# Kernel optimization log

Hardware: AMD Instinct MI355X
Metric: run time of the kernel (lower is better)

The kernel has to match this reference:

```python
import jax, jax.numpy as jnp
import numpy as np
from jax import lax

P = 32   # patch_size
D = 128  # emb_dim
E = 8    # num_experts
K = 2    # top-k
C = 3    # in_channels


def _conv(x, w, b, stride, groups, pad):
    y = lax.conv_general_dilated(
        x, w, (stride, stride), [(pad, pad), (pad, pad)],
        feature_group_count=groups,
        dimension_numbers=('NCHW', 'OIHW', 'NCHW'))
    return jax.nn.relu(y + b[None, :, None, None])


def setup_inputs() -> dict:
    key = jax.random.key(0)
    ks = jax.random.split(key, 16)
    s = 0.02
    inp = {
        'x': jax.random.normal(ks[0], (16, C, 512, 512), dtype=jnp.float32),
        'gate_w1': jax.random.normal(ks[1], (C * P * P, D), dtype=jnp.float32) * s,
        'gate_b1': jnp.zeros((D,), jnp.float32),
        'gate_w2': jax.random.normal(ks[2], (D, E), dtype=jnp.float32) * s,
        'gate_b2': jnp.zeros((E,), jnp.float32),
        'dw1_w': jax.random.normal(ks[3], (E, C, 1, 3, 3), dtype=jnp.float32) * s,
        'dw1_b': jnp.zeros((E, C), jnp.float32),
        'pw1_w': jax.random.normal(ks[4], (E, D, C, 1, 1), dtype=jnp.float32) * s,
        'pw1_b': jnp.zeros((E, D), jnp.float32),
        'dw2_w': jax.random.normal(ks[5], (E, D, 1, 3, 3), dtype=jnp.float32) * s,
        'dw2_b': jnp.zeros((E, D), jnp.float32),
        'pw2_w': jax.random.normal(ks[6], (E, D, D, 1, 1), dtype=jnp.float32) * s,
        'pw2_b': jnp.zeros((E, D), jnp.float32),
    }
    return inp


def reference(x, gate_w1, gate_b1, gate_w2, gate_b2,
              dw1_w, dw1_b, pw1_w, pw1_b, dw2_w, dw2_b, pw2_w, pw2_b):
    B, Cc, H, W = x.shape
    hp, wp = H // P, W // P
    N = hp * wp
    BN = B * N
    # nn.Unfold(kernel=stride=P) -> non-overlapping patches, (c,i,j) flatten order
    patches = x.reshape(B, Cc, hp, P, wp, P)
    patches = patches.transpose(0, 2, 4, 1, 3, 5).reshape(B, N, Cc * P * P)
    # gate MLP
    h = jax.nn.relu(patches @ gate_w1 + gate_b1)
    logits = h @ gate_w2 + gate_b2              # [B,N,E]
    topk_vals, topk_idx = lax.top_k(logits, K)  # sorted descending, like torch
    weights = jax.nn.softmax(topk_vals, axis=-1)
    patches_sp = patches.reshape(BN, Cc, P, P)
    # dense per-expert depthwise-separable conv stacks (small fixed loop over E)
    outs = []
    for e in range(E):
        y = _conv(patches_sp, dw1_w[e], dw1_b[e], 2, Cc, 1)  # [BN,C,16,16]
        y = _conv(y, pw1_w[e], pw1_b[e], 1, 1, 0)            # [BN,D,16,16]
        y = _conv(y, dw2_w[e], dw2_b[e], 2, D, 1)            # [BN,D,8,8]
        y = _conv(y, pw2_w[e], pw2_b[e], 1, 1, 0)            # [BN,D,8,8]
        outs.append(y.mean(axis=(2, 3)))                     # adaptive avg pool 1
    expert_outs = jnp.stack(outs, axis=1)                    # [BN,E,D]
    idx = topk_idx.reshape(BN, K)
    w = weights.reshape(BN, K)
    sel = jnp.take_along_axis(expert_outs, idx[:, :, None], axis=1)  # [BN,K,D]
    out = (w[:, :, None] * sel).sum(axis=1)                  # [BN,D]
    return out.reshape(B, hp, wp, D).transpose(0, 3, 1, 2)
```

## Files before the change

kernel.cpp:

```cpp
#include <hip/hip_runtime.h>

#define NPATCH 4096
#define NFRAG 49152

typedef __attribute__((ext_vector_type(8))) __bf16 bf16x8;
typedef __attribute__((ext_vector_type(4))) __bf16 bf16x4;
typedef __attribute__((ext_vector_type(4))) float f32x4;

__global__ __launch_bounds__(256) void prep_kernel(const float* __restrict__ pw2_w,
                                                   bf16x8* __restrict__ wpk) {
  int tid = blockIdx.x * 256 + threadIdx.x;
  int l = tid & 63, nt = (tid >> 6) & 7, kt = (tid >> 9) & 3, e = tid >> 11;
  int n = nt * 16 + (l & 15);
  int k = kt * 32 + (l >> 4) * 8;
  const float* src = &pw2_w[((size_t)(e * 128 + n)) * 128 + k];
  float4 a = *(const float4*)src;
  float4 b = *(const float4*)(src + 4);
  bf16x8 r = { (__bf16)a.x, (__bf16)a.y, (__bf16)a.z, (__bf16)a.w,
               (__bf16)b.x, (__bf16)b.y, (__bf16)b.z, (__bf16)b.w };
  wpk[tid] = r;
}

__global__ __launch_bounds__(256) void prep_w1(const float* __restrict__ w1,
                                               bf16x8* __restrict__ w1f) {
  int tid = blockIdx.x * 256 + threadIdx.x;
  int l = tid & 63, nt = (tid >> 6) & 7, ktg = tid >> 9;
  int k0 = ktg * 32 + (l >> 4) * 8, d = nt * 16 + (l & 15);
  bf16x8 h, lo;
#pragma unroll
  for (int j = 0; j < 8; ++j) {
    float v = w1[(size_t)(k0 + j) * 128 + d];
    __bf16 hv = (__bf16)v;
    h[j] = hv;
    lo[j] = (__bf16)(v - (float)hv);
  }
  w1f[tid] = h;
  w1f[NFRAG + tid] = lo;
}

__global__ __launch_bounds__(512) void gate_mfma(
    const float* __restrict__ x, const bf16x8* __restrict__ w1f,
    const float* __restrict__ b1, const float* __restrict__ w2,
    const float* __restrict__ b2, int* __restrict__ gidx,
    float* __restrict__ gw)
{
  __shared__ __bf16 Ah[2][8][64][8];
  __shared__ __bf16 Al[2][8][64][8];
  __shared__ float hs[16][128];
  __shared__ float ls[16][8];

  const int t  = threadIdx.x;
  const int p0 = blockIdx.x * 16;
  const int l  = t & 63;
  const int wv = t >> 6;
  const int mrow  = l & 15;
  const int kslot = l >> 4;

  const int sp   = l & 15;
  const int sj4  = (l >> 4) + 4 * (wv & 1);
  const int srr0 = (wv >> 1);
  const int srr1 = 4 + (wv >> 1);
  size_t pbase;
  {
    int gp = p0 + sp;
    int bb = gp >> 8, ph = (gp >> 4) & 15, pwc = gp & 15;
    pbase = ((size_t)(bb * 3) * 512 + ph * 32) * 512 + pwc * 32;
  }

  f32x4 accA[4], accB[4];
#pragma unroll
  for (int i = 0; i < 4; ++i) {
    accA[i] = (f32x4){0.f, 0.f, 0.f, 0.f};
    accB[i] = (f32x4){0.f, 0.f, 0.f, 0.f};
  }

#define SLOAD(ch, R0, R1) do {                                                      \
    R0 = *(const float4*)&x[pbase + (size_t)((ch) >> 2) * 262144 +                  \
                            (size_t)(((ch) & 3) * 8 + srr0) * 512 + sj4 * 4];       \
    R1 = *(const float4*)&x[pbase + (size_t)((ch) >> 2) * 262144 +                  \
                            (size_t)(((ch) & 3) * 8 + srr1) * 512 + sj4 * 4];       \
  } while (0)

#define SPLIT4(V, HP, LP) do {                                                      \
    bf16x4 h_, lo_;                                                                 \
    h_[0] = (__bf16)V.x; lo_[0] = (__bf16)(V.x - (float)h_[0]);                     \
    h_[1] = (__bf16)V.y; lo_[1] = (__bf16)(V.y - (float)h_[1]);                     \
    h_[2] = (__bf16)V.z; lo_[2] = (__bf16)(V.z - (float)h_[2]);                     \
    h_[3] = (__bf16)V.w; lo_[3] = (__bf16)(V.w - (float)h_[3]);                     \
    *(bf16x4*)(HP) = h_; *(bf16x4*)(LP) = lo_;                                      \
  } while (0)

#define SSTORE(ch, R0, R1) do {                                                     \
    const int bf_ = (ch) & 1;                                                       \
    SPLIT4(R0, &Ah[bf_][srr0][(sj4 >> 1) * 16 + sp][(sj4 & 1) * 4],                 \
               &Al[bf_][srr0][(sj4 >> 1) * 16 + sp][(sj4 & 1) * 4]);                \
    SPLIT4(R1, &Ah[bf_][srr1][(sj4 >> 1) * 16 + sp][(sj4 & 1) * 4],                 \
               &Al[bf_][srr1][(sj4 >> 1) * 16 + sp][(sj4 & 1) * 4]);                \
  } while (0)

#define BLOAD(ch, BH, BL) do {                                                      \
    const bf16x8* wp_ = w1f + (size_t)(ch) * 4096 + wv * 64 + l;                    \
    _Pragma("unroll")                                                               \
    for (int q = 0; q < 8; ++q) { BH[q] = wp_[q * 512]; BL[q] = wp_[NFRAG + q * 512]; } \
  } while (0)

#define MFMA_PASS(ch, BH, BL) do {                                                  \
    const int bf_ = (ch) & 1;                                                       \
    _Pragma("unroll")                                                               \
    for (int ktl = 0; ktl < 8; ++ktl) {                                             \
      bf16x8 ah_ = *(const bf16x8*)&Ah[bf_][ktl][l][0];                             \
      bf16x8 al_ = *(const bf16x8*)&Al[bf_][ktl][l][0];                             \
      const int r_ = ktl & 3;                                                       \
      accA[r_] = __builtin_amdgcn_mfma_f32_16x16x32_bf16(ah_, BH[ktl], accA[r_], 0, 0, 0); \
      accB[r_] = __builtin_amdgcn_mfma_f32_16x16x32_bf16(ah_, BL[ktl], accB[r_], 0, 0, 0); \
      accB[r_] = __builtin_amdgcn_mfma_f32_16x16x32_bf16(al_, BH[ktl], accB[r_], 0, 0, 0); \
    }                                                                               \
  } while (0)

  float4 r0, r1;
  bf16x8 bh0[8], bl0[8], bh1[8], bl1[8];

  SLOAD(0, r0, r1);
  BLOAD(0, bh0, bl0);
  SSTORE(0, r0, r1);
  __syncthreads();

#pragma unroll
  for (int cc = 0; cc < 12; cc += 2) {
    if (cc + 1 < 12) { SLOAD(cc + 1, r0, r1); BLOAD(cc + 1, bh1, bl1); }
    MFMA_PASS(cc, bh0, bl0);
    if (cc + 1 < 12) SSTORE(cc + 1, r0, r1);
    __syncthreads();
    if (cc + 2 < 12) { SLOAD(cc + 2, r0, r1); BLOAD(cc + 2, bh0, bl0); }
    MFMA_PASS(cc + 1, bh1, bl1);
    if (cc + 2 < 12) SSTORE(cc + 2, r0, r1);
    __syncthreads();
  }
#undef SLOAD
#undef SPLIT4
#undef SSTORE
#undef BLOAD
#undef MFMA_PASS

  {
    f32x4 sA = (accA[0] + accA[1]) + (accA[2] + accA[3]);
    f32x4 sB = (accB[0] + accB[1]) + (accB[2] + accB[3]);
    const int d = wv * 16 + mrow;
    const float bb1 = b1[d];
#pragma unroll
    for (int r = 0; r < 4; ++r) {
      int m = kslot * 4 + r;
      hs[m][d] = fmaxf(sA[r] + sB[r] + bb1, 0.f);
    }
  }
  __syncthreads();

  if (t < 128) {
    int p = t >> 3, e = t & 7;
    float s = 0.f;
    for (int d0 = 0; d0 < 128; d0 += 32) {
      float cs = 0.f;
#pragma unroll
      for (int dd = 0; dd < 32; ++dd)
        cs = fmaf(hs[p][d0 + dd], w2[(d0 + dd) * 8 + e], cs);
      s += cs;
    }
    ls[p][e] = s + b2[e];
  }
  __syncthreads();

  if (t < 16) {
    int gp = p0 + t;
    float v[8];
#pragma unroll
    for (int e = 0; e < 8; ++e) v[e] = ls[t][e];
    int e0 = 0;
#pragma unroll
    for (int e = 1; e < 8; ++e) if (v[e] > v[e0]) e0 = e;
    int e1 = (e0 == 0) ? 1 : 0;
#pragma unroll
    for (int e = 0; e < 8; ++e) { if (e != e0 && v[e] > v[e1]) e1 = e; }
    float bexp = expf(v[e1] - v[e0]);
    float inv  = 1.f / (1.f + bexp);
    gidx[gp * 2 + 0] = e0;
    gidx[gp * 2 + 1] = e1;
    gw[gp * 2 + 0] = inv;
    gw[gp * 2 + 1] = bexp * inv;
  }
}

__global__ __launch_bounds__(512, 4) void gate_kernel(
    const float* __restrict__ x, const float* __restrict__ w1,
    const float* __restrict__ b1, const float* __restrict__ w2,
    const float* __restrict__ b2, int* __restrict__ gidx,
    float* __restrict__ gw)
{
  __shared__ float As[8][1024];
  __shared__ float hs[8][128];
  __shared__ float ls[8][8];

  const int t   = threadIdx.x;
  const int p0  = blockIdx.x * 8;
  const int d   = t & 127;
  const int grp = t >> 7;
  const int pa  = grp * 2, pb = grp * 2 + 1;

  float acc0 = 0.f, acc1 = 0.f;

  for (int c = 0; c < 3; ++c) {
#pragma unroll
    for (int it = 0; it < 4; ++it) {
      int i = t + it * 512;
      int p = i >> 8, rem = i & 255, r = rem >> 3, j4 = (rem & 7) * 4;
      int gp = p0 + p;
      int bb = gp >> 8, ph = (gp >> 4) & 15, pwc = gp & 15;
      *(float4*)&As[p][r * 32 + j4] =
          *(const float4*)&x[((size_t)(bb * 3 + c) * 512 + ph * 32 + r) * 512 + pwc * 32 + j4];
    }
    __syncthreads();

    const float* wdp = w1 + (size_t)c * 131072 + d;
    for (int ch = 0; ch < 32; ++ch) {
      float bv[32];
#pragma unroll
      for (int j = 0; j < 32; ++j) bv[j] = wdp[(ch * 32 + j) * 128];
      const int kl = ch * 32;
      float ca = 0.f, cb = 0.f;
#pragma unroll
      for (int q = 0; q < 8; ++q) {
        float4 a0 = *(const float4*)&As[pa][kl + q * 4];
        float4 a1 = *(const float4*)&As[pb][kl + q * 4];
        ca = fmaf(a0.x, bv[q * 4 + 0], ca); ca = fmaf(a0.y, bv[q * 4 + 1], ca);
        ca = fmaf(a0.z, bv[q * 4 + 2], ca); ca = fmaf(a0.w, bv[q * 4 + 3], ca);
        cb = fmaf(a1.x, bv[q * 4 + 0], cb); cb = fmaf(a1.y, bv[q * 4 + 1], cb);
        cb = fmaf(a1.z, bv[q * 4 + 2], cb); cb = fmaf(a1.w, bv[q * 4 + 3], cb);
      }
      acc0 += ca; acc1 += cb;
    }
    __syncthreads();
  }

  hs[pa][d] = fmaxf(acc0 + b1[d], 0.f);
  hs[pb][d] = fmaxf(acc1 + b1[d], 0.f);
  __syncthreads();

  if (t < 64) {
    int p = t >> 3, e = t & 7;
    float s = 0.f;
    for (int d0 = 0; d0 < 128; d0 += 32) {
      float cs = 0.f;
#pragma unroll
      for (int dd = 0; dd < 32; ++dd)
        cs = fmaf(hs[p][d0 + dd], w2[(d0 + dd) * 8 + e], cs);
      s += cs;
    }
    ls[p][e] = s + b2[e];
  }
  __syncthreads();

  if (t < 8) {
    int gp = p0 + t;
    float v[8];
#pragma unroll
    for (int e = 0; e < 8; ++e) v[e] = ls[t][e];
    int e0 = 0;
#pragma unroll
    for (int e = 1; e < 8; ++e) if (v[e] > v[e0]) e0 = e;
    int e1 = (e0 == 0) ? 1 : 0;
#pragma unroll
    for (int e = 0; e < 8; ++e) { if (e != e0 && v[e] > v[e1]) e1 = e; }
    float bexp = expf(v[e1] - v[e0]);
    float inv  = 1.f / (1.f + bexp);
    gidx[gp * 2 + 0] = e0;
    gidx[gp * 2 + 1] = e1;
    gw[gp * 2 + 0] = inv;
    gw[gp * 2 + 1] = bexp * inv;
  }
}


#define EXPERT_COMMON_PRE                                                          \
  __shared__ float  ps[3][32][36];                                                 \
  __shared__ float  y1s[3][256];                                                   \
  __shared__ __bf16 y3b[64][140];                                                  \
  __shared__ float  posum[4][128];                                                 \
  __shared__ float  outbuf[128];                                                   \
  const int t  = threadIdx.x;                                                      \
  const int gp = blockIdx.x;                                                       \
  const int b = gp >> 8, ph = (gp >> 4) & 15, pw = gp & 15;                        \
  const int l = t & 63, wv = t >> 6;                                               \
  _Pragma("unroll")                                                                \
  for (int it = 0; it < 3; ++it) {                                                 \
    int f4i = t + 256 * it;                                                        \
    int c = f4i >> 8, r = (f4i >> 3) & 31, j4 = f4i & 7;                           \
    *(float4*)&ps[c][r][j4 * 4] =                                                  \
        *(const float4*)&x[((size_t)(b * 3 + c) * 512 + ph * 32 + r) * 512 +       \
                           pw * 32 + j4 * 4];                                      \
  }                                                                                \
  if (t < 128) outbuf[t] = 0.f;                                                    \
  const int dd   = t & 127;                                                        \
  const int half = t >> 7;                                                         \
  __syncthreads();

#define EXPERT_PHASES_1_2                                                          \
    for (int oi = t; oi < 768; oi += 256) {                                        \
      int c = oi >> 8, p = (oi >> 4) & 15, q = oi & 15;                            \
      float a = dw1_b[e * 3 + c];                                                  \
      const float* wp_ = &dw1_w[(e * 3 + c) * 9];                                  \
      _Pragma("unroll")                                                            \
      for (int di = 0; di < 3; ++di) {                                             \
        int ii = 2 * p + di - 1;                                                   \
        if (ii < 0) continue;                                                      \
        _Pragma("unroll")                                                          \
        for (int dj = 0; dj < 3; ++dj) {                                           \
          int jj = 2 * q + dj - 1;                                                 \
          if (jj < 0) continue;                                                    \
          a = fmaf(wp_[di * 3 + dj], ps[c][ii][jj], a);                            \
        }                                                                          \
      }                                                                            \
      y1s[c][p * 16 + q] = fmaxf(a, 0.f);                                          \
    }                                                                              \
    __syncthreads();                                                               \
    {                                                                              \
      const float pwa = pw1_w[(e * 128 + dd) * 3 + 0];                             \
      const float pwb = pw1_w[(e * 128 + dd) * 3 + 1];                             \
      const float pwc = pw1_w[(e * 128 + dd) * 3 + 2];                             \
      const float pb  = pw1_b[e * 128 + dd];                                       \
      float dwv[9];                                                                \
      _Pragma("unroll")                                                            \
      for (int i = 0; i < 9; ++i) dwv[i] = dw2_w[(e * 128 + dd) * 9 + i];          \
      const float db = dw2_b[e * 128 + dd];                                        \
      for (int u = half * 4; u < half * 4 + 4; ++u) {                              \
        float vacc[8];                                                             \
        _Pragma("unroll")                                                          \
        for (int v = 0; v < 8; ++v) vacc[v] = db;                                  \
        _Pragma("unroll")                                                          \
        for (int di = 0; di < 3; ++di) {                                           \
          int ii = 2 * u + di - 1;                                                 \
          if (ii < 0) continue;                                                    \
          float y2row[16];                                                         \
          _Pragma("unroll")                                                        \
          for (int q4 = 0; q4 < 4; ++q4) {                                         \
            float4 a  = *(const float4*)&y1s[0][ii * 16 + q4 * 4];                 \
            float4 bq = *(const float4*)&y1s[1][ii * 16 + q4 * 4];                 \
            float4 cq = *(const float4*)&y1s[2][ii * 16 + q4 * 4];                 \
            y2row[q4 * 4 + 0] = fmaxf(fmaf(pwa, a.x, fmaf(pwb, bq.x, fmaf(pwc, cq.x, pb))), 0.f); \
            y2row[q4 * 4 + 1] = fmaxf(fmaf(pwa, a.y, fmaf(pwb, bq.y, fmaf(pwc, cq.y, pb))), 0.f); \
            y2row[q4 * 4 + 2] = fmaxf(fmaf(pwa, a.z, fmaf(pwb, bq.z, fmaf(pwc, cq.z, pb))), 0.f); \
            y2row[q4 * 4 + 3] = fmaxf(fmaf(pwa, a.w, fmaf(pwb, bq.w, fmaf(pwc, cq.w, pb))), 0.f); \
          }                                                                        \
          _Pragma("unroll")                                                        \
          for (int v = 0; v < 8; ++v) {                                            \
            _Pragma("unroll")                                                      \
            for (int dj = 0; dj < 3; ++dj) {                                       \
              int jj = 2 * v + dj - 1;                                             \
              if (jj < 0) continue;                                                \
              vacc[v] = fmaf(dwv[di * 3 + dj], y2row[jj], vacc[v]);                \
            }                                                                      \
          }                                                                        \
        }                                                                          \
        _Pragma("unroll")                                                          \
        for (int v = 0; v < 8; ++v)                                                \
          y3b[u * 8 + v][dd] = (__bf16)fmaxf(vacc[v], 0.f);                        \
      }                                                                            \
    }

#define EXPERT_EPILOG                                                              \
    _Pragma("unroll")                                                              \
    for (int nt = 0; nt < 8; ++nt) {                                               \
      float bias = pw2_b[e * 128 + nt * 16 + (l & 15)];                            \
      float s = fmaxf(acc[nt][0] + bias, 0.f) + fmaxf(acc[nt][1] + bias, 0.f)      \
              + fmaxf(acc[nt][2] + bias, 0.f) + fmaxf(acc[nt][3] + bias, 0.f);     \
      s += __shfl_xor(s, 16);                                                      \
      s += __shfl_xor(s, 32);                                                      \
      if (l < 16) posum[wv][nt * 16 + l] = s;                                      \
    }

__global__ __launch_bounds__(256, 4) void expert_packed(
    const float* __restrict__ x,
    const float* __restrict__ dw1_w, const float* __restrict__ dw1_b,
    const float* __restrict__ pw1_w, const float* __restrict__ pw1_b,
    const float* __restrict__ dw2_w, const float* __restrict__ dw2_b,
    const bf16x8* __restrict__ wpk, const float* __restrict__ pw2_b,
    const int* __restrict__ gidx, const float* __restrict__ gw,
    float* __restrict__ out)
{
  EXPERT_COMMON_PRE
  for (int k = 0; k < 2; ++k) {
    const int   e  = gidx[gp * 2 + k];
    const float wk = gw[gp * 2 + k];
    EXPERT_PHASES_1_2
    __syncthreads();
    {
      f32x4 acc[8];
#pragma unroll
      for (int nt = 0; nt < 8; ++nt) acc[nt] = (f32x4){0.f, 0.f, 0.f, 0.f};
      const int row  = wv * 16 + (l & 15);
      const int kofs = (l >> 4) * 8;
      bf16x8 afrag[4];
#pragma unroll
      for (int kt = 0; kt < 4; ++kt)
        afrag[kt] = *(const bf16x8*)&y3b[row][kt * 32 + kofs];
      const bf16x8* wb = wpk + (size_t)e * 2048 + l;
#pragma unroll
      for (int kt = 0; kt < 4; ++kt) {
        bf16x8 bf[8];
#pragma unroll
        for (int nt = 0; nt < 8; ++nt) bf[nt] = wb[(kt * 8 + nt) * 64];
#pragma unroll
        for (int nt = 0; nt < 8; ++nt)
          acc[nt] = __builtin_amdgcn_mfma_f32_16x16x32_bf16(afrag[kt], bf[nt], acc[nt], 0, 0, 0);
      }
      EXPERT_EPILOG
    }
    __syncthreads();
    if (t < 128)
      outbuf[t] += wk * 0.015625f *
                   (posum[0][t] + posum[1][t] + posum[2][t] + posum[3][t]);
    __syncthreads();
  }
  if (t < 128)
    out[((size_t)(b * 128 + t) * 16 + ph) * 16 + pw] = outbuf[t];
}

__global__ __launch_bounds__(256) void expert_fb(
    const float* __restrict__ x,
    const float* __restrict__ dw1_w, const float* __restrict__ dw1_b,
    const float* __restrict__ pw1_w, const float* __restrict__ pw1_b,
    const float* __restrict__ dw2_w, const float* __restrict__ dw2_b,
    const float* __restrict__ pw2_w, const float* __restrict__ pw2_b,
    const int* __restrict__ gidx, const float* __restrict__ gw,
    float* __restrict__ out)
{
  __shared__ __bf16 wlds[128][136];
  EXPERT_COMMON_PRE
  for (int k = 0; k < 2; ++k) {
    const int   e  = gidx[gp * 2 + k];
    const float wk = gw[gp * 2 + k];
    EXPERT_PHASES_1_2
    for (int i4 = t; i4 < 4096; i4 += 256) {
      int n = i4 >> 5, kq = i4 & 31;
      float4 w4 = *(const float4*)&pw2_w[((size_t)(e * 128 + n)) * 128 + kq * 4];
      bf16x4 pk = { (__bf16)w4.x, (__bf16)w4.y, (__bf16)w4.z, (__bf16)w4.w };
      *(bf16x4*)&wlds[n][kq * 4] = pk;
    }
    __syncthreads();
    {
      f32x4 acc[8];
#pragma unroll
      for (int nt = 0; nt < 8; ++nt) acc[nt] = (f32x4){0.f, 0.f, 0.f, 0.f};
      const int row  = wv * 16 + (l & 15);
      const int kofs = (l >> 4) * 8;
      bf16x8 afrag[4];
#pragma unroll
      for (int kt = 0; kt < 4; ++kt)
        afrag[kt] = *(const bf16x8*)&y3b[row][kt * 32 + kofs];
#pragma unroll
      for (int kt = 0; kt < 4; ++kt) {
#pragma unroll
        for (int nt = 0; nt < 8; ++nt) {
          bf16x8 bfrag = *(const bf16x8*)&wlds[nt * 16 + (l & 15)][kt * 32 + kofs];
          acc[nt] = __builtin_amdgcn_mfma_f32_16x16x32_bf16(afrag[kt], bfrag, acc[nt], 0, 0, 0);
        }
      }
      EXPERT_EPILOG
    }
    __syncthreads();
    if (t < 128)
      outbuf[t] += wk * 0.015625f *
                   (posum[0][t] + posum[1][t] + posum[2][t] + posum[3][t]);
    __syncthreads();
  }
  if (t < 128)
    out[((size_t)(b * 128 + t) * 16 + ph) * 16 + pw] = outbuf[t];
}

extern "C" void kernel_launch(void* const* d_in, const int* in_sizes, int n_in,
                              void* d_out, int out_size, void* d_ws, size_t ws_size,
                              hipStream_t stream) {
  const float* x       = (const float*)d_in[0];
  const float* gate_w1 = (const float*)d_in[1];
  const float* gate_b1 = (const float*)d_in[2];
  const float* gate_w2 = (const float*)d_in[3];
  const float* gate_b2 = (const float*)d_in[4];
  const float* dw1_w   = (const float*)d_in[5];
  const float* dw1_b   = (const float*)d_in[6];
  const float* pw1_w   = (const float*)d_in[7];
  const float* pw1_b   = (const float*)d_in[8];
  const float* dw2_w   = (const float*)d_in[9];
  const float* dw2_b   = (const float*)d_in[10];
  const float* pw2_w   = (const float*)d_in[11];
  const float* pw2_b   = (const float*)d_in[12];
  float* out = (float*)d_out;

  int*    gidx = (int*)d_ws;
  float*  gw   = (float*)((char*)d_ws + (size_t)NPATCH * 2 * sizeof(int));
  bf16x8* wpk  = (bf16x8*)((char*)d_ws + (size_t)NPATCH * 4 * sizeof(int));
  bf16x8* w1f  = (bf16x8*)((char*)d_ws + (size_t)NPATCH * 4 * sizeof(int) + 256 * 1024);
  const size_t ws_pack = (size_t)NPATCH * 4 * sizeof(int) + 256 * 1024;
  const size_t ws_full = ws_pack + (size_t)NFRAG * 2 * 16;
  const bool packed = ws_size >= ws_pack;
  const bool mfgate = ws_size >= ws_full;

  if (mfgate) {
    prep_w1<<<192, 256, 0, stream>>>(gate_w1, w1f);
    gate_mfma<<<NPATCH / 16, 512, 0, stream>>>(x, w1f, gate_b1, gate_w2, gate_b2, gidx, gw);
  } else {
    gate_kernel<<<NPATCH / 8, 512, 0, stream>>>(x, gate_w1, gate_b1, gate_w2, gate_b2, gidx, gw);
  }
  if (packed) {
    prep_kernel<<<64, 256, 0, stream>>>(pw2_w, wpk);
    expert_packed<<<NPATCH, 256, 0, stream>>>(x, dw1_w, dw1_b, pw1_w, pw1_b,
                                              dw2_w, dw2_b, wpk, pw2_b, gidx, gw, out);
  } else {
    expert_fb<<<NPATCH, 256, 0, stream>>>(x, dw1_w, dw1_b, pw1_w, pw1_b,
                                          dw2_w, dw2_b, pw2_w, pw2_b, gidx, gw, out);
  }
}
```

Before: 247.9 us.

## Split gate GEMM along K across two blocks with a separate logits kernel

The gate MLP's first GEMM is split into two K halves, each handled by its own block, so the grid grows from 256 to 512 blocks. Partial hidden sums go to a workspace buffer, and a new gate_logits kernel adds them, applies bias and ReLU, then computes logits and top-2 softmax. The aim is to fill more CUs during the gate phase, since 256 blocks underfill the GPU. The cost is an extra launch and a 4 MB partial-sum round trip through global memory, and the path only runs when the workspace is large enough.

New measurement: 246.5 us. Within noise of the previous version (-0.6%).

```diff
diff --git a/kernel.cpp b/kernel.cpp
--- a/kernel.cpp
+++ b/kernel.cpp
@@ -38,41 +38,16 @@
   w1f[NFRAG + tid] = lo;
 }
 
-__global__ __launch_bounds__(512) void gate_mfma(
-    const float* __restrict__ x, const bf16x8* __restrict__ w1f,
-    const float* __restrict__ b1, const float* __restrict__ w2,
-    const float* __restrict__ b2, int* __restrict__ gidx,
-    float* __restrict__ gw)
-{
-  __shared__ __bf16 Ah[2][8][64][8];
-  __shared__ __bf16 Al[2][8][64][8];
-  __shared__ float hs[16][128];
-  __shared__ float ls[16][8];
-
-  const int t  = threadIdx.x;
-  const int p0 = blockIdx.x * 16;
-  const int l  = t & 63;
-  const int wv = t >> 6;
-  const int mrow  = l & 15;
-  const int kslot = l >> 4;
-
-  const int sp   = l & 15;
-  const int sj4  = (l >> 4) + 4 * (wv & 1);
-  const int srr0 = (wv >> 1);
+#define GATE_DECLS                                                                  \
+  const int t  = threadIdx.x;                                                       \
+  const int l  = t & 63;                                                            \
+  const int wv = t >> 6;                                                            \
+  const int mrow  = l & 15;                                                         \
+  const int kslot = l >> 4;                                                         \
+  const int sp   = l & 15;                                                          \
+  const int sj4  = (l >> 4) + 4 * (wv & 1);                                         \
+  const int srr0 = (wv >> 1);                                                       \
   const int srr1 = 4 + (wv >> 1);
-  size_t pbase;
-  {
-    int gp = p0 + sp;
-    int bb = gp >> 8, ph = (gp >> 4) & 15, pwc = gp & 15;
-    pbase = ((size_t)(bb * 3) * 512 + ph * 32) * 512 + pwc * 32;
-  }
-
-  f32x4 accA[4], accB[4];
-#pragma unroll
-  for (int i = 0; i < 4; ++i) {
-    accA[i] = (f32x4){0.f, 0.f, 0.f, 0.f};
-    accB[i] = (f32x4){0.f, 0.f, 0.f, 0.f};
-  }
 
 #define SLOAD(ch, R0, R1) do {                                                      \
     R0 = *(const float4*)&x[pbase + (size_t)((ch) >> 2) * 262144 +                  \
@@ -117,6 +92,144 @@
     }                                                                               \
   } while (0)
 
+__global__ __launch_bounds__(512) void gate_mfma_split(
+    const float* __restrict__ x, const bf16x8* __restrict__ w1f,
+    float* __restrict__ hpart)
+{
+  __shared__ __bf16 Ah[2][8][64][8];
+  __shared__ __bf16 Al[2][8][64][8];
+
+  GATE_DECLS
+  const int kh = blockIdx.x & 1;
+  const int p0 = (blockIdx.x >> 1) * 16;
+  const int cb = kh * 6;
+
+  size_t pbase;
+  {
+    int gp = p0 + sp;
+    int bb = gp >> 8, ph = (gp >> 4) & 15, pwc = gp & 15;
+    pbase = ((size_t)(bb * 3) * 512 + ph * 32) * 512 + pwc * 32;
+  }
+
+  f32x4 accA[4], accB[4];
+#pragma unroll
+  for (int i = 0; i < 4; ++i) {
+    accA[i] = (f32x4){0.f, 0.f, 0.f, 0.f};
+    accB[i] = (f32x4){0.f, 0.f, 0.f, 0.f};
+  }
+
+  float4 r0, r1;
+  bf16x8 bh0[8], bl0[8], bh1[8], bl1[8];
+
+  SLOAD(cb + 0, r0, r1);
+  BLOAD(cb + 0, bh0, bl0);
+  SSTORE(cb + 0, r0, r1);
+  __syncthreads();
+
+#pragma unroll
+  for (int cc = 0; cc < 6; cc += 2) {
+    if (cc + 1 < 6) { SLOAD(cb + cc + 1, r0, r1); BLOAD(cb + cc + 1, bh1, bl1); }
+    MFMA_PASS(cb + cc, bh0, bl0);
+    if (cc + 1 < 6) SSTORE(cb + cc + 1, r0, r1);
+    __syncthreads();
+    if (cc + 2 < 6) { SLOAD(cb + cc + 2, r0, r1); BLOAD(cb + cc + 2, bh0, bl0); }
+    MFMA_PASS(cb + cc + 1, bh1, bl1);
+    if (cc + 2 < 6) SSTORE(cb + cc + 2, r0, r1);
+    __syncthreads();
+  }
+
+  {
+    f32x4 sA = (accA[0] + accA[1]) + (accA[2] + accA[3]);
+    f32x4 sB = (accB[0] + accB[1]) + (accB[2] + accB[3]);
+    const int d = wv * 16 + mrow;
+#pragma unroll
+    for (int r = 0; r < 4; ++r) {
+      int m = kslot * 4 + r;
+      hpart[((size_t)kh * NPATCH + p0 + m) * 128 + d] = sA[r] + sB[r];
+    }
+  }
+}
+
+__global__ __launch_bounds__(256) void gate_logits(
+    const float* __restrict__ hpart, const float* __restrict__ b1,
+    const float* __restrict__ w2, const float* __restrict__ b2,
+    int* __restrict__ gidx, float* __restrict__ gw)
+{
+  __shared__ float hs[16][128];
+  __shared__ float ls[16][8];
+  const int t  = threadIdx.x;
+  const int p0 = blockIdx.x * 16;
+
+  for (int i = t; i < 2048; i += 256) {
+    int p = i >> 7, d = i & 127;
+    float h0 = hpart[((size_t)(p0 + p)) * 128 + d];
+    float h1 = hpart[((size_t)NPATCH + p0 + p) * 128 + d];
+    hs[p][d] = fmaxf((h0 + h1) + b1[d], 0.f);
+  }
+  __syncthreads();
+
+  if (t < 128) {
+    int p = t >> 3, e = t & 7;
+    float s = 0.f;
+    for (int d0 = 0; d0 < 128; d0 += 32) {
+      float cs = 0.f;
+#pragma unroll
+      for (int dd = 0; dd < 32; ++dd)
+        cs = fmaf(hs[p][d0 + dd], w2[(d0 + dd) * 8 + e], cs);
+      s += cs;
+    }
+    ls[p][e] = s + b2[e];
+  }
+  __syncthreads();
+
+  if (t < 16) {
+    int gp = p0 + t;
+    float v[8];
+#pragma unroll
+    for (int e = 0; e < 8; ++e) v[e] = ls[t][e];
+    int e0 = 0;
+#pragma unroll
+    for (int e = 1; e < 8; ++e) if (v[e] > v[e0]) e0 = e;
+    int e1 = (e0 == 0) ? 1 : 0;
+#pragma unroll
+    for (int e = 0; e < 8; ++e) { if (e != e0 && v[e] > v[e1]) e1 = e; }
+    float bexp = expf(v[e1] - v[e0]);
+    float inv  = 1.f / (1.f + bexp);
+    gidx[gp * 2 + 0] = e0;
+    gidx[gp * 2 + 1] = e1;
+    gw[gp * 2 + 0] = inv;
+    gw[gp * 2 + 1] = bexp * inv;
+  }
+}
+
+__global__ __launch_bounds__(512) void gate_mfma(
+    const float* __restrict__ x, const bf16x8* __restrict__ w1f,
+    const float* __restrict__ b1, const float* __restrict__ w2,
+    const float* __restrict__ b2, int* __restrict__ gidx,
+    float* __restrict__ gw)
+{
+  __shared__ __bf16 Ah[2][8][64][8];
+  __shared__ __bf16 Al[2][8][64][8];
+  __shared__ float hs[16][128];
+  __shared__ float ls[16][8];
+
+  GATE_DECLS
+  const int p0 = blockIdx.x * 16;
+
+  size_t pbase;
+  {
+    int gp = p0 + sp;
+    int bb = gp >> 8, ph = (gp >> 4) & 15, pwc = gp & 15;
+    pbase = ((size_t)(bb * 3) * 512 + ph * 32) * 512 + pwc * 32;
+  }
+
+  f32x4 accA[4], accB[4];
+#pragma unroll
+  for (int i = 0; i < 4; ++i) {
+    accA[i] = (f32x4){0.f, 0.f, 0.f, 0.f};
+    accB[i] = (f32x4){0.f, 0.f, 0.f, 0.f};
+  }
+
   float4 r0, r1;
   bf16x8 bh0[8], bl0[8], bh1[8], bl1[8];
 
@@ -136,11 +249,6 @@
     if (cc + 2 < 12) SSTORE(cc + 2, r0, r1);
     __syncthreads();
   }
-#undef SLOAD
-#undef SPLIT4
-#undef SSTORE
-#undef BLOAD
-#undef MFMA_PASS
 
   {
     f32x4 sA = (accA[0] + accA[1]) + (accA[2] + accA[3]);
@@ -277,7 +385,6 @@
     gw[gp * 2 + 1] = bexp * inv;
   }
 }
-
 
 #define EXPERT_COMMON_PRE                                                          \
   __shared__ float  ps[3][32][36];                                                 \
@@ -493,16 +600,28 @@
   const float* pw2_b   = (const float*)d_in[12];
   float* out = (float*)d_out;
 
-  int*    gidx = (int*)d_ws;
-  float*  gw   = (float*)((char*)d_ws + (size_t)NPATCH * 2 * sizeof(int));
-  bf16x8* wpk  = (bf16x8*)((char*)d_ws + (size_t)NPATCH * 4 * sizeof(int));
-  bf16x8* w1f  = (bf16x8*)((char*)d_ws + (size_t)NPATCH * 4 * sizeof(int) + 256 * 1024);
-  const size_t ws_pack = (size_t)NPATCH * 4 * sizeof(int) + 256 * 1024;
-  const size_t ws_full = ws_pack + (size_t)NFRAG * 2 * 16;
-  const bool packed = ws_size >= ws_pack;
-  const bool mfgate = ws_size >= ws_full;
-
-  if (mfgate) {
+  const size_t off_wpk   = (size_t)NPATCH * 4 * sizeof(int);
+  const size_t off_w1f   = off_wpk + 256 * 1024;
+  const size_t off_hpart = off_w1f + (size_t)NFRAG * 2 * 16;
+  const size_t ws_pack   = off_w1f;
+  const size_t ws_full   = off_hpart;
+  const size_t ws_split  = off_hpart + (size_t)2 * NPATCH * 128 * sizeof(float);
+
+  int*    gidx  = (int*)d_ws;
+  float*  gw    = (float*)((char*)d_ws + (size_t)NPATCH * 2 * sizeof(int));
+  bf16x8* wpk   = (bf16x8*)((char*)d_ws + off_wpk);
+  bf16x8* w1f   = (bf16x8*)((char*)d_ws + off_w1f);
+  float*  hpart = (float*)((char*)d_ws + off_hpart);
+
+  const bool packed  = ws_size >= ws_pack;
+  const bool mfgate  = ws_size >= ws_full;
+  const bool splitk  = ws_size >= ws_split;
+
+  if (splitk) {
+    prep_w1<<<192, 256, 0, stream>>>(gate_w1, w1f);
+    gate_mfma_split<<<512, 512, 0, stream>>>(x, w1f, hpart);
+    gate_logits<<<NPATCH / 16, 256, 0, stream>>>(hpart, gate_b1, gate_w2, gate_b2, gidx, gw);
+  } else if (mfgate) {
     prep_w1<<<192, 256, 0, stream>>>(gate_w1, w1f);
     gate_mfma<<<NPATCH / 16, 512, 0, stream>>>(x, w1f, gate_b1, gate_w2, gate_b2, gidx, gw);
   } else {
```
